# Performance work log

Hardware: AMD Instinct MI355X
Metric: run time of the kernel (lower is better)

The kernel has to match this reference:

```python
import jax, jax.numpy as jnp
import numpy as np
from jax import lax

K = 3          # kernel size
PAD = 1        # 'same' padding for k=3: (1,1,1,1)
STRIDE = 1
DIL = 1
OFFSET_SIZE = 2 * K * K  # deformable_groups=1


def setup_inputs() -> dict:
    key = jax.random.key(0)
    k1, k2, k3, k4 = jax.random.split(key, 4)
    B, H, W, C = 8, 64, 64, 256
    F = 256
    inputs = jax.random.normal(k1, (B, H, W, C), dtype=jnp.float32)
    # offset/mask branch conv: small weights so sampled offsets are modest
    om_kernel = jax.random.normal(k2, (K, K, C, OFFSET_SIZE * 3 // 2), dtype=jnp.float32) * 0.01
    om_bias = jnp.zeros((OFFSET_SIZE * 3 // 2,), dtype=jnp.float32)
    stdv = 1.0 / np.sqrt(K * K * C)
    kernel = jax.random.uniform(k3, (K * K * C, F), dtype=jnp.float32, minval=-stdv, maxval=stdv)
    bias = jax.random.normal(k4, (1, 1, 1, F), dtype=jnp.float32) * 0.01
    return {"inputs": inputs, "om_kernel": om_kernel, "om_bias": om_bias,
            "kernel": kernel, "bias": bias}


def _dcnv2(x, om_kernel, om_bias, kernel, bias):
    B, H, W, C = x.shape
    # offset/mask branch (same conv geometry as the deformable conv)
    om = lax.conv_general_dilated(
        x, om_kernel, window_strides=(STRIDE, STRIDE),
        padding=((PAD, PAD), (PAD, PAD)), rhs_dilation=(DIL, DIL),
        dimension_numbers=('NHWC', 'HWIO', 'NHWC')) + om_bias
    OH, OW = om.shape[1], om.shape[2]
    KK = K * K
    offset = om[..., :OFFSET_SIZE].reshape(B, OH, OW, KK, 2)  # (dy, dx) per kernel point
    mask = jax.nn.sigmoid(om[..., OFFSET_SIZE:]) * 2.0         # [B,OH,OW,KK]

    # base sampling grid per output pixel and kernel point
    kk = jnp.arange(KK)
    ky = (kk // K).astype(jnp.float32)
    kx = (kk % K).astype(jnp.float32)
    base_y = jnp.arange(OH, dtype=jnp.float32)[:, None] * STRIDE - PAD + ky[None, :] * DIL  # [OH,KK]
    base_x = jnp.arange(OW, dtype=jnp.float32)[:, None] * STRIDE - PAD + kx[None, :] * DIL  # [OW,KK]

    py = base_y[None, :, None, :] + offset[..., 0]  # [B,OH,OW,KK]
    px = base_x[None, None, :, :] + offset[..., 1]

    y0 = jnp.floor(py); x0 = jnp.floor(px)
    wy1 = py - y0; wy0 = 1.0 - wy1
    wx1 = px - x0; wx0 = 1.0 - wx1

    bi = jnp.arange(B)[:, None, None, None]

    def gather(yi, xi):
        # zero-padded bilinear corner fetch
        valid = (yi >= 0) & (yi <= H - 1) & (xi >= 0) & (xi <= W - 1)
        yc = jnp.clip(yi, 0, H - 1).astype(jnp.int32)
        xc = jnp.clip(xi, 0, W - 1).astype(jnp.int32)
        v = x[bi, yc, xc]  # [B,OH,OW,KK,C]
        return v * valid[..., None].astype(x.dtype)

    y1 = y0 + 1.0; x1 = x0 + 1.0
    cols = (gather(y0, x0) * (wy0 * wx0)[..., None]
            + gather(y0, x1) * (wy0 * wx1)[..., None]
            + gather(y1, x0) * (wy1 * wx0)[..., None]
            + gather(y1, x1) * (wy1 * wx1)[..., None])
    cols = cols * mask[..., None]  # modulation, [B,OH,OW,KK,C]

    out = cols.reshape(B, OH, OW, KK * C) @ kernel  # [B,OH,OW,F]
    return out + bias


def reference(inputs, om_kernel, om_bias, kernel, bias):
    return _dcnv2(inputs, om_kernel, om_bias, kernel, bias)
```

## Files before the change

kernel.cpp:

```cpp
#include <hip/hip_runtime.h>
#include <math.h>


#define BB 8
#define HH 64
#define WW 64
#define CIN 256
#define FF 256
#define KPTS 9
#define OCH 27
#define MT 32
#define KSTEPS 72
#define AST 40

typedef _Float16 half8  __attribute__((ext_vector_type(8)));
typedef _Float16 half4v __attribute__((ext_vector_type(4)));
typedef float    floatx4 __attribute__((ext_vector_type(4)));

__global__ __launch_bounds__(256) void convert_wmat(const float* __restrict__ wmat,
                                                    _Float16* __restrict__ wsB) {
    const int kg = blockIdx.x;
    const int n  = threadIdx.x;
    half8 h;
    #pragma unroll
    for (int j = 0; j < 8; ++j)
        h[j] = (_Float16)wmat[(size_t)(kg * 8 + j) * FF + n];
    ((half8*)wsB)[(size_t)kg * FF + n] = h;
}

__global__ __launch_bounds__(256) void convert_omw(const float* __restrict__ omw,
                                                   _Float16* __restrict__ wsOM) {
    const int t = blockIdx.x * 256 + threadIdx.x;
    const int k = t >> 5, n = t & 31;
    const float v = (n < OCH) ? omw[k * OCH + n] : 0.f;
    wsOM[((size_t)(k >> 3) * 32 + n) * 8 + (k & 7)] = (_Float16)v;
}

__global__ __launch_bounds__(256) void dcn_mfma(
    const float* __restrict__ x,
    const float* __restrict__ omb,
    const _Float16* __restrict__ wsB,
    const _Float16* __restrict__ wsOM,
    const float* __restrict__ bias,
    float* __restrict__ out)
{
    __shared__ _Float16 Ah0[MT * AST];
    __shared__ _Float16 Ah1[MT * AST];
    __shared__ float    om_s[MT][28];
    __shared__ floatx4  cwS[MT][KPTS];
    __shared__ int4     caS[MT][KPTS];

    const int tid  = threadIdx.x;
    const int w    = tid >> 6;
    const int lane = tid & 63;
    const int q    = lane >> 4;
    const int lr   = lane & 15;

    const int p   = blockIdx.x;
    const int b   = p & 7;
    const int r2  = p >> 3;
    const int oh  = r2 >> 1;
    const int owb = (r2 & 1) * 32;
    const int pbase = (b * HH + oh) * WW + owb;

    const int mrow = tid >> 3;
    const int cg   = tid & 7;

    const half8* wsOM8 = (const half8*)wsOM;
    const half8* wsB8  = (const half8*)wsB;

    const int mt1 = w & 1;
    const int nt1 = w >> 1;
    floatx4 acc1 = {0.f, 0.f, 0.f, 0.f};

    auto pre1 = [&](int s2, floatx4& cA, half8& bPre) {
        const int kk = s2 >> 3, cb = (s2 & 7) << 5;
        const int ky = kk / 3, kx = kk % 3;
        const int iy = oh - 1 + ky, ix = owb + mrow - 1 + kx;
        floatx4 v = {0.f, 0.f, 0.f, 0.f};
        if (iy >= 0 && iy < HH && ix >= 0 && ix < WW)
            v = *(const floatx4*)(x + ((size_t)((b * HH + iy) * WW + ix) * CIN + cb + cg * 4));
        cA = v;
        bPre = wsOM8[(s2 * 4 + q) * 32 + nt1 * 16 + lr];
    };

    floatx4 cA0, cA1;
    half8 bo0, bo1;
    pre1(0, cA0, bo0);
    for (int s = 0; s < KSTEPS; s += 2) {
        {
            half4v hv;
            hv.x = (_Float16)cA0.x; hv.y = (_Float16)cA0.y;
            hv.z = (_Float16)cA0.z; hv.w = (_Float16)cA0.w;
            *(half4v*)(&Ah0[mrow * AST + cg * 4]) = hv;
            pre1(s + 1, cA1, bo1);
            __syncthreads();
            const half8 a = *(const half8*)(&Ah0[(mt1 * 16 + lr) * AST + q * 8]);
            acc1 = __builtin_amdgcn_mfma_f32_16x16x32_f16(a, bo0, acc1, 0, 0, 0);
        }
        {
            half4v hv;
            hv.x = (_Float16)cA1.x; hv.y = (_Float16)cA1.y;
            hv.z = (_Float16)cA1.z; hv.w = (_Float16)cA1.w;
            *(half4v*)(&Ah1[mrow * AST + cg * 4]) = hv;
            const int s2 = (s + 2 < KSTEPS) ? s + 2 : KSTEPS - 1;
            pre1(s2, cA0, bo0);
            __syncthreads();
            const half8 a = *(const half8*)(&Ah1[(mt1 * 16 + lr) * AST + q * 8]);
            acc1 = __builtin_amdgcn_mfma_f32_16x16x32_f16(a, bo1, acc1, 0, 0, 0);
        }
    }
    {
        const int och = nt1 * 16 + lr;
        if (och < OCH) {
            const float ob = omb[och];
            #pragma unroll
            for (int reg = 0; reg < 4; ++reg) {
                const int m = mt1 * 16 + q * 4 + reg;
                om_s[m][och] = acc1[reg] + ob;
            }
        }
    }
    __syncthreads();

    for (int i = tid; i < MT * KPTS; i += 256) {
        const int m = i / KPTS, kk = i % KPTS;
        const int ky = kk / 3, kx = kk % 3;
        const float dy = om_s[m][2 * kk];
        const float dx = om_s[m][2 * kk + 1];
        const float mask = 2.f / (1.f + __expf(-om_s[m][18 + kk]));
        const float py = (float)(oh - 1 + ky) + dy;
        const float px = (float)(owb + m - 1 + kx) + dx;
        const float y0f = floorf(py), x0f = floorf(px);
        const float wy1 = py - y0f, wx1 = px - x0f;
        const float wy0 = 1.f - wy1, wx0 = 1.f - wx1;
        const int y0 = (int)y0f, x0 = (int)x0f;
        const int y1 = y0 + 1, x1 = x0 + 1;
        const bool vy0 = (y0 >= 0) && (y0 < HH);
        const bool vy1 = (y1 >= 0) && (y1 < HH);
        const bool vx0 = (x0 >= 0) && (x0 < WW);
        const bool vx1 = (x1 >= 0) && (x1 < WW);
        const int y0c = min(max(y0, 0), HH - 1), y1c = min(max(y1, 0), HH - 1);
        const int x0c = min(max(x0, 0), WW - 1), x1c = min(max(x1, 0), WW - 1);
        const int rb = b * HH;
        int4 ca;
        ca.x = ((rb + y0c) * WW + x0c) * CIN;
        ca.y = ((rb + y0c) * WW + x1c) * CIN;
        ca.z = ((rb + y1c) * WW + x0c) * CIN;
        ca.w = ((rb + y1c) * WW + x1c) * CIN;
        floatx4 cw;
        cw.x = (vy0 && vx0) ? mask * wy0 * wx0 : 0.f;
        cw.y = (vy0 && vx1) ? mask * wy0 * wx1 : 0.f;
        cw.z = (vy1 && vx0) ? mask * wy1 * wx0 : 0.f;
        cw.w = (vy1 && vx1) ? mask * wy1 * wx1 : 0.f;
        caS[m][kk] = ca;
        cwS[m][kk] = cw;
    }
    __syncthreads();

    floatx4 acc[2][4];
    #pragma unroll
    for (int mt = 0; mt < 2; ++mt)
        #pragma unroll
        for (int nt = 0; nt < 4; ++nt)
            acc[mt][nt] = (floatx4){0.f, 0.f, 0.f, 0.f};

    const int n0w = w * 64;

    auto pre2 = [&](int s2, floatx4& c0, floatx4& c1, floatx4& c2, floatx4& c3,
                    floatx4& cw, half8 (&bP)[4]) {
        const int kk2 = s2 >> 3;
        const int4 ca = caS[mrow][kk2];
        cw = cwS[mrow][kk2];
        const int co = ((s2 & 7) << 5) + cg * 4;
        c0 = *(const floatx4*)(x + ca.x + co);
        c1 = *(const floatx4*)(x + ca.y + co);
        c2 = *(const floatx4*)(x + ca.z + co);
        c3 = *(const floatx4*)(x + ca.w + co);
        #pragma unroll
        for (int nt = 0; nt < 4; ++nt)
            bP[nt] = wsB8[(s2 * 4 + q) * FF + n0w + nt * 16 + lr];
    };

    floatx4 ca0, ca1, ca2, ca3, cwa;
    floatx4 cb0, cb1, cb2, cb3, cwb;
    half8 bPa[4], bPb[4];
    pre2(0, ca0, ca1, ca2, ca3, cwa, bPa);

    for (int s = 0; s < KSTEPS; s += 2) {
        {
            const floatx4 v = cwa.x * ca0 + cwa.y * ca1 + cwa.z * ca2 + cwa.w * ca3;
            half4v hv;
            hv.x = (_Float16)v.x; hv.y = (_Float16)v.y;
            hv.z = (_Float16)v.z; hv.w = (_Float16)v.w;
            *(half4v*)(&Ah0[mrow * AST + cg * 4]) = hv;
            pre2(s + 1, cb0, cb1, cb2, cb3, cwb, bPb);
            __syncthreads();
            const half8 a0 = *(const half8*)(&Ah0[lr * AST + q * 8]);
            const half8 a1 = *(const half8*)(&Ah0[(16 + lr) * AST + q * 8]);
            #pragma unroll
            for (int nt = 0; nt < 4; ++nt) {
                acc[0][nt] = __builtin_amdgcn_mfma_f32_16x16x32_f16(a0, bPa[nt], acc[0][nt], 0, 0, 0);
                acc[1][nt] = __builtin_amdgcn_mfma_f32_16x16x32_f16(a1, bPa[nt], acc[1][nt], 0, 0, 0);
            }
        }
        {
            const floatx4 v = cwb.x * cb0 + cwb.y * cb1 + cwb.z * cb2 + cwb.w * cb3;
            half4v hv;
            hv.x = (_Float16)v.x; hv.y = (_Float16)v.y;
            hv.z = (_Float16)v.z; hv.w = (_Float16)v.w;
            *(half4v*)(&Ah1[mrow * AST + cg * 4]) = hv;
            const int s2 = (s + 2 < KSTEPS) ? s + 2 : KSTEPS - 1;
            pre2(s2, ca0, ca1, ca2, ca3, cwa, bPa);
            __syncthreads();
            const half8 a0 = *(const half8*)(&Ah1[lr * AST + q * 8]);
            const half8 a1 = *(const half8*)(&Ah1[(16 + lr) * AST + q * 8]);
            #pragma unroll
            for (int nt = 0; nt < 4; ++nt) {
                acc[0][nt] = __builtin_amdgcn_mfma_f32_16x16x32_f16(a0, bPb[nt], acc[0][nt], 0, 0, 0);
                acc[1][nt] = __builtin_amdgcn_mfma_f32_16x16x32_f16(a1, bPb[nt], acc[1][nt], 0, 0, 0);
            }
        }
    }

    #pragma unroll
    for (int nt = 0; nt < 4; ++nt) {
        const int f = n0w + nt * 16 + lr;
        const float bv = bias[f];
        #pragma unroll
        for (int mt = 0; mt < 2; ++mt)
            #pragma unroll
            for (int reg = 0; reg < 4; ++reg) {
                const int m = mt * 16 + q * 4 + reg;
                out[(size_t)(pbase + m) * FF + f] = acc[mt][nt][reg] + bv;
            }
    }
}

#define MTILE 32
#define CHUNK 64
#define NCHUNK (CIN / CHUNK)

__global__ __launch_bounds__(256) void dcn_fused(
    const float* __restrict__ x, const float* __restrict__ omw,
    const float* __restrict__ omb, const float* __restrict__ wmat,
    const float* __restrict__ bias, float* __restrict__ out)
{
    __shared__ float A[CHUNK][MTILE + 1];
    __shared__ float om_s[MTILE][28];
    __shared__ float cw[MTILE][4];
    __shared__ int   ca[MTILE][4];

    const int tid = threadIdx.x;
    const int pbase = blockIdx.x * MTILE;
    const int ccid = tid & 63;
    const int mg2 = tid >> 6;
    const int och = tid & 31;
    const int mg1 = tid >> 5;
    float acc1[4] = {0.f, 0.f, 0.f, 0.f};

    for (int kk = 0; kk < KPTS; ++kk) {
        const int ky = kk / 3, kx = kk % 3;
        for (int ch = 0; ch < NCHUNK; ++ch) {
            const int cbase = ch * CHUNK;
            __syncthreads();
            #pragma unroll
            for (int i = 0; i < 8; ++i) {
                const int m = mg2 * 8 + i;
                const int pp = pbase + m;
                const int bb = pp >> 12, oh = (pp >> 6) & 63, ow = pp & 63;
                const int iy = oh - 1 + ky, ix = ow - 1 + kx;
                float v = 0.f;
                if (iy >= 0 && iy < HH && ix >= 0 && ix < WW)
                    v = x[((bb * HH + iy) * WW + ix) * CIN + cbase + ccid];
                A[ccid][m] = v;
            }
            __syncthreads();
            if (och < OCH) {
                for (int cc = 0; cc < CHUNK; ++cc) {
                    const float bv = omw[((kk * CIN) + cbase + cc) * OCH + och];
                    #pragma unroll
                    for (int i = 0; i < 4; ++i)
                        acc1[i] += A[cc][mg1 * 4 + i] * bv;
                }
            }
        }
    }
    __syncthreads();
    if (och < OCH) {
        const float ob = omb[och];
        #pragma unroll
        for (int i = 0; i < 4; ++i)
            om_s[mg1 * 4 + i][och] = acc1[i] + ob;
    }
    __syncthreads();

    const int f4 = (tid & 63) * 4;
    const int mgc = tid >> 6;
    float acc[8][4];
    #pragma unroll
    for (int j = 0; j < 8; ++j)
        #pragma unroll
        for (int i = 0; i < 4; ++i) acc[j][i] = 0.f;

    for (int kk = 0; kk < KPTS; ++kk) {
        if (tid < MTILE) {
            const int m = tid;
            const int pp = pbase + m;
            const int bb = pp >> 12, oh = (pp >> 6) & 63, ow = pp & 63;
            const int ky = kk / 3, kx = kk % 3;
            const float dy = om_s[m][2 * kk];
            const float dx = om_s[m][2 * kk + 1];
            const float mask = 2.f / (1.f + __expf(-om_s[m][18 + kk]));
            const float py = (float)(oh - 1 + ky) + dy;
            const float px = (float)(ow - 1 + kx) + dx;
            const float y0f = floorf(py), x0f = floorf(px);
            const float wy1 = py - y0f, wx1 = px - x0f;
            const float wy0 = 1.f - wy1, wx0 = 1.f - wx1;
            const int y0 = (int)y0f, x0 = (int)x0f;
            const int y1 = y0 + 1, x1 = x0 + 1;
            const bool vy0 = (y0 >= 0) && (y0 < HH);
            const bool vy1 = (y1 >= 0) && (y1 < HH);
            const bool vx0 = (x0 >= 0) && (x0 < WW);
            const bool vx1 = (x1 >= 0) && (x1 < WW);
            const int y0c = min(max(y0, 0), HH - 1), y1c = min(max(y1, 0), HH - 1);
            const int x0c = min(max(x0, 0), WW - 1), x1c = min(max(x1, 0), WW - 1);
            const int rb = bb * HH;
            ca[m][0] = ((rb + y0c) * WW + x0c) * CIN;
            ca[m][1] = ((rb + y0c) * WW + x1c) * CIN;
            ca[m][2] = ((rb + y1c) * WW + x0c) * CIN;
            ca[m][3] = ((rb + y1c) * WW + x1c) * CIN;
            cw[m][0] = (vy0 && vx0) ? mask * wy0 * wx0 : 0.f;
            cw[m][1] = (vy0 && vx1) ? mask * wy0 * wx1 : 0.f;
            cw[m][2] = (vy1 && vx0) ? mask * wy1 * wx0 : 0.f;
            cw[m][3] = (vy1 && vx1) ? mask * wy1 * wx1 : 0.f;
        }
        for (int ch = 0; ch < NCHUNK; ++ch) {
            const int cbase = ch * CHUNK;
            __syncthreads();
            #pragma unroll
            for (int i = 0; i < 8; ++i) {
                const int m = mg2 * 8 + i;
                const int cidx = cbase + ccid;
                const float v = cw[m][0] * x[ca[m][0] + cidx]
                              + cw[m][1] * x[ca[m][1] + cidx]
                              + cw[m][2] * x[ca[m][2] + cidx]
                              + cw[m][3] * x[ca[m][3] + cidx];
                A[ccid][m] = v;
            }
            __syncthreads();
            const float* brow = wmat + (size_t)(kk * CIN + cbase) * FF + f4;
            for (int cc = 0; cc < CHUNK; ++cc) {
                const float4 bv = *(const float4*)(brow + cc * FF);
                #pragma unroll
                for (int j = 0; j < 8; ++j) {
                    const float a = A[cc][mgc * 8 + j];
                    acc[j][0] += a * bv.x;
                    acc[j][1] += a * bv.y;
                    acc[j][2] += a * bv.z;
                    acc[j][3] += a * bv.w;
                }
            }
        }
    }

    const float4 bb4 = *(const float4*)(bias + f4);
    #pragma unroll
    for (int j = 0; j < 8; ++j) {
        const int m = mgc * 8 + j;
        const int pp = pbase + m;
        float4 o;
        o.x = acc[j][0] + bb4.x;
        o.y = acc[j][1] + bb4.y;
        o.z = acc[j][2] + bb4.z;
        o.w = acc[j][3] + bb4.w;
        *(float4*)(out + (size_t)pp * FF + f4) = o;
    }
}

extern "C" void kernel_launch(void* const* d_in, const int* in_sizes, int n_in,
                              void* d_out, int out_size, void* d_ws, size_t ws_size,
                              hipStream_t stream) {
    const float* x    = (const float*)d_in[0];
    const float* omw  = (const float*)d_in[1];
    const float* omb  = (const float*)d_in[2];
    const float* wmat = (const float*)d_in[3];
    const float* bias = (const float*)d_in[4];
    float* out = (float*)d_out;

    const size_t needB  = (size_t)2304 * FF * sizeof(_Float16);
    const size_t needOM = (size_t)288 * 32 * 8 * sizeof(_Float16);

    if (ws_size >= needB + needOM) {
        _Float16* wsB  = (_Float16*)d_ws;
        _Float16* wsOM = (_Float16*)((char*)d_ws + needB);
        convert_wmat<<<288, 256, 0, stream>>>(wmat, wsB);
        convert_omw<<<288, 256, 0, stream>>>(omw, wsOM);
        dcn_mfma<<<BB * HH * 2, 256, 0, stream>>>(x, omb, wsB, wsOM, bias, out);
    } else {
        const int nblocks = (BB * HH * WW) / MTILE;
        dcn_fused<<<nblocks, 256, 0, stream>>>(x, omw, omb, wmat, bias, out);
    }
}
```

Before: 192.0 us.

## Use 512-thread full-row tiles with warp-group producer split, f16 input copy, swizzled LDS

Each block now covers a full output row of 64 pixels with 512 threads. The two 256-thread halves alternately fill the two LDS A buffers while all warps run MFMA, which lets gather latency overlap compute. A pre-pass converts x to fp16 in the workspace so the bilinear gathers fetch half the bytes, and the bilinear blend is done in fp16. LDS rows use an XOR swizzle instead of padding. The fp16 blending and weights lower accuracy, and the extra conversion pass of x adds a full read and write of the input.

```diff
diff --git a/kernel.cpp b/kernel.cpp
--- a/kernel.cpp
+++ b/kernel.cpp
@@ -9,13 +9,32 @@
 #define FF 256
 #define KPTS 9
 #define OCH 27
-#define MT 32
+#define MT 64
 #define KSTEPS 72
-#define AST 40
 
 typedef _Float16 half8  __attribute__((ext_vector_type(8)));
 typedef _Float16 half4v __attribute__((ext_vector_type(4)));
 typedef float    floatx4 __attribute__((ext_vector_type(4)));
+
+__device__ __forceinline__ int aoff(int m, int g) {
+    return m * 32 + ((g ^ ((m >> 1) & 3)) << 3);
+}
+
+__device__ __forceinline__ half8 splat8(_Float16 v) {
+    half8 r = {v, v, v, v, v, v, v, v};
+    return r;
+}
+
+__global__ __launch_bounds__(256) void convert_x(const float* __restrict__ x,
+                                                 _Float16* __restrict__ xh) {
+    const size_t i = ((size_t)blockIdx.x * 256 + threadIdx.x) * 8;
+    const floatx4 a = *(const floatx4*)(x + i);
+    const floatx4 b = *(const floatx4*)(x + i + 4);
+    half8 h;
+    h[0] = (_Float16)a.x; h[1] = (_Float16)a.y; h[2] = (_Float16)a.z; h[3] = (_Float16)a.w;
+    h[4] = (_Float16)b.x; h[5] = (_Float16)b.y; h[6] = (_Float16)b.z; h[7] = (_Float16)b.w;
+    *(half8*)(xh + i) = h;
+}
 
 __global__ __launch_bounds__(256) void convert_wmat(const float* __restrict__ wmat,
                                                     _Float16* __restrict__ wsB) {
@@ -36,18 +55,20 @@
     wsOM[((size_t)(k >> 3) * 32 + n) * 8 + (k & 7)] = (_Float16)v;
 }
 
-__global__ __launch_bounds__(256) void dcn_mfma(
+template <bool F16X>
+__global__ __launch_bounds__(512) void dcn_mfma2(
     const float* __restrict__ x,
+    const _Float16* __restrict__ xh,
     const float* __restrict__ omb,
     const _Float16* __restrict__ wsB,
     const _Float16* __restrict__ wsOM,
     const float* __restrict__ bias,
     float* __restrict__ out)
 {
-    __shared__ _Float16 Ah0[MT * AST];
-    __shared__ _Float16 Ah1[MT * AST];
+    __shared__ _Float16 Ah0[MT * 32];
+    __shared__ _Float16 Ah1[MT * 32];
     __shared__ float    om_s[MT][28];
-    __shared__ floatx4  cwS[MT][KPTS];
+    __shared__ half4v   cwS[MT][KPTS];
     __shared__ int4     caS[MT][KPTS];
 
     const int tid  = threadIdx.x;
@@ -55,58 +76,80 @@
     const int lane = tid & 63;
     const int q    = lane >> 4;
     const int lr   = lane & 15;
-
-    const int p   = blockIdx.x;
-    const int b   = p & 7;
-    const int r2  = p >> 3;
-    const int oh  = r2 >> 1;
-    const int owb = (r2 & 1) * 32;
-    const int pbase = (b * HH + oh) * WW + owb;
-
-    const int mrow = tid >> 3;
-    const int cg   = tid & 7;
+    const int g    = tid >> 8;
+    const int st   = tid & 255;
+    const int ms   = st >> 2;
+    const int qc   = st & 3;
+
+    const int p  = blockIdx.x;
+    const int b  = p & 7;
+    const int oh = p >> 3;
+    const int pbase = (b * HH + oh) * WW;
 
     const half8* wsOM8 = (const half8*)wsOM;
     const half8* wsB8  = (const half8*)wsB;
 
-    const int mt1 = w & 1;
-    const int nt1 = w >> 1;
+    const int mt1 = w & 3;
+    const int nt1 = w >> 2;
     floatx4 acc1 = {0.f, 0.f, 0.f, 0.f};
 
-    auto pre1 = [&](int s2, floatx4& cA, half8& bPre) {
-        const int kk = s2 >> 3, cb = (s2 & 7) << 5;
-        const int ky = kk / 3, kx = kk % 3;
-        const int iy = oh - 1 + ky, ix = owb + mrow - 1 + kx;
-        floatx4 v = {0.f, 0.f, 0.f, 0.f};
-        if (iy >= 0 && iy < HH && ix >= 0 && ix < WW)
-            v = *(const floatx4*)(x + ((size_t)((b * HH + iy) * WW + ix) * CIN + cb + cg * 4));
-        cA = v;
-        bPre = wsOM8[(s2 * 4 + q) * 32 + nt1 * 16 + lr];
+    auto load1 = [&](int sp) -> half8 {
+        sp = sp < KSTEPS - 1 ? sp : KSTEPS - 1;
+        const int kk = sp >> 3, cb = (sp & 7) << 5;
+        const int ky = kk / 3, kx = kk - ky * 3;
+        const int iy = oh - 1 + ky, ix = ms - 1 + kx;
+        half8 v = {(_Float16)0, (_Float16)0, (_Float16)0, (_Float16)0,
+                   (_Float16)0, (_Float16)0, (_Float16)0, (_Float16)0};
+        if (iy >= 0 && iy < HH && ix >= 0 && ix < WW) {
+            const int idx = ((b * HH + iy) * WW + ix) * CIN + cb + qc * 8;
+            if constexpr (F16X) {
+                v = *(const half8*)(xh + idx);
+            } else {
+                const floatx4 lo = *(const floatx4*)(x + idx);
+                const floatx4 hi = *(const floatx4*)(x + idx + 4);
+                v[0] = (_Float16)lo.x; v[1] = (_Float16)lo.y;
+                v[2] = (_Float16)lo.z; v[3] = (_Float16)lo.w;
+                v[4] = (_Float16)hi.x; v[5] = (_Float16)hi.y;
+                v[6] = (_Float16)hi.z; v[7] = (_Float16)hi.w;
+            }
+        }
+        return v;
     };
-
-    floatx4 cA0, cA1;
+    auto loadB1 = [&](int sp) -> half8 {
+        sp = sp < KSTEPS - 1 ? sp : KSTEPS - 1;
+        return wsOM8[(sp * 4 + q) * 32 + nt1 * 16 + lr];
+    };
+
+    half8 vp1;
     half8 bo0, bo1;
-    pre1(0, cA0, bo0);
+    if (g == 0) {
+        const half8 v0 = load1(0);
+        *(half8*)(Ah0 + aoff(ms, qc)) = v0;
+        vp1 = load1(2);
+    } else {
+        vp1 = load1(1);
+    }
+    bo0 = loadB1(0);
+
     for (int s = 0; s < KSTEPS; s += 2) {
+        __syncthreads();
+        if (g == 1) {
+            *(half8*)(Ah1 + aoff(ms, qc)) = vp1;
+            vp1 = load1(s + 3);
+        }
+        bo1 = loadB1(s + 1);
         {
-            half4v hv;
-            hv.x = (_Float16)cA0.x; hv.y = (_Float16)cA0.y;
-            hv.z = (_Float16)cA0.z; hv.w = (_Float16)cA0.w;
-            *(half4v*)(&Ah0[mrow * AST + cg * 4]) = hv;
-            pre1(s + 1, cA1, bo1);
-            __syncthreads();
-            const half8 a = *(const half8*)(&Ah0[(mt1 * 16 + lr) * AST + q * 8]);
+            const half8 a = *(const half8*)(Ah0 + aoff(mt1 * 16 + lr, q));
             acc1 = __builtin_amdgcn_mfma_f32_16x16x32_f16(a, bo0, acc1, 0, 0, 0);
         }
+        __syncthreads();
+        if (g == 0) {
+            *(half8*)(Ah0 + aoff(ms, qc)) = vp1;
+            vp1 = load1(s + 4);
+        }
+        bo0 = loadB1(s + 2);
         {
-            half4v hv;
-            hv.x = (_Float16)cA1.x; hv.y = (_Float16)cA1.y;
-            hv.z = (_Float16)cA1.z; hv.w = (_Float16)cA1.w;
-            *(half4v*)(&Ah1[mrow * AST + cg * 4]) = hv;
-            const int s2 = (s + 2 < KSTEPS) ? s + 2 : KSTEPS - 1;
-            pre1(s2, cA0, bo0);
-            __syncthreads();
-            const half8 a = *(const half8*)(&Ah1[(mt1 * 16 + lr) * AST + q * 8]);
+            const half8 a = *(const half8*)(Ah1 + aoff(mt1 * 16 + lr, q));
             acc1 = __builtin_amdgcn_mfma_f32_16x16x32_f16(a, bo1, acc1, 0, 0, 0);
         }
     }
@@ -123,14 +166,14 @@
     }
     __syncthreads();
 
-    for (int i = tid; i < MT * KPTS; i += 256) {
+    for (int i = tid; i < MT * KPTS; i += 512) {
         const int m = i / KPTS, kk = i % KPTS;
-        const int ky = kk / 3, kx = kk % 3;
+        const int ky = kk / 3, kx = kk - ky * 3;
         const float dy = om_s[m][2 * kk];
         const float dx = om_s[m][2 * kk + 1];
         const float mask = 2.f / (1.f + __expf(-om_s[m][18 + kk]));
         const float py = (float)(oh - 1 + ky) + dy;
-        const float px = (float)(owb + m - 1 + kx) + dx;
+        const float px = (float)(m - 1 + kx) + dx;
         const float y0f = floorf(py), x0f = floorf(px);
         const float wy1 = py - y0f, wx1 = px - x0f;
         const float wy0 = 1.f - wy1, wx0 = 1.f - wx1;
@@ -148,87 +191,129 @@
         ca.y = ((rb + y0c) * WW + x1c) * CIN;
         ca.z = ((rb + y1c) * WW + x0c) * CIN;
         ca.w = ((rb + y1c) * WW + x1c) * CIN;
-        floatx4 cw;
-        cw.x = (vy0 && vx0) ? mask * wy0 * wx0 : 0.f;
-        cw.y = (vy0 && vx1) ? mask * wy0 * wx1 : 0.f;
-        cw.z = (vy1 && vx0) ? mask * wy1 * wx0 : 0.f;
-        cw.w = (vy1 && vx1) ? mask * wy1 * wx1 : 0.f;
+        half4v cw;
+        cw.x = (_Float16)((vy0 && vx0) ? mask * wy0 * wx0 : 0.f);
+        cw.y = (_Float16)((vy0 && vx1) ? mask * wy0 * wx1 : 0.f);
+        cw.z = (_Float16)((vy1 && vx0) ? mask * wy1 * wx0 : 0.f);
+        cw.w = (_Float16)((vy1 && vx1) ? mask * wy1 * wx1 : 0.f);
         caS[m][kk] = ca;
         cwS[m][kk] = cw;
     }
     __syncthreads();
 
-    floatx4 acc[2][4];
+    floatx4 acc[4][2];
     #pragma unroll
-    for (int mt = 0; mt < 2; ++mt)
+    for (int mt = 0; mt < 4; ++mt)
         #pragma unroll
-        for (int nt = 0; nt < 4; ++nt)
+        for (int nt = 0; nt < 2; ++nt)
             acc[mt][nt] = (floatx4){0.f, 0.f, 0.f, 0.f};
 
-    const int n0w = w * 64;
-
-    auto pre2 = [&](int s2, floatx4& c0, floatx4& c1, floatx4& c2, floatx4& c3,
-                    floatx4& cw, half8 (&bP)[4]) {
-        const int kk2 = s2 >> 3;
-        const int4 ca = caS[mrow][kk2];
-        cw = cwS[mrow][kk2];
-        const int co = ((s2 & 7) << 5) + cg * 4;
-        c0 = *(const floatx4*)(x + ca.x + co);
-        c1 = *(const floatx4*)(x + ca.y + co);
-        c2 = *(const floatx4*)(x + ca.z + co);
-        c3 = *(const floatx4*)(x + ca.w + co);
+    const int n0w = w * 32;
+
+    half8   pc0, pc1, pc2, pc3;
+    floatx4 fa0, fb0, fa1, fb1, fa2, fb2, fa3, fb3;
+    half4v  pcw;
+
+    auto pre2 = [&](int sp) {
+        sp = sp < KSTEPS - 1 ? sp : KSTEPS - 1;
+        const int kk = sp >> 3;
+        const int co = ((sp & 7) << 5) + qc * 8;
+        const int4 ca = caS[ms][kk];
+        pcw = cwS[ms][kk];
+        if constexpr (F16X) {
+            pc0 = *(const half8*)(xh + ca.x + co);
+            pc1 = *(const half8*)(xh + ca.y + co);
+            pc2 = *(const half8*)(xh + ca.z + co);
+            pc3 = *(const half8*)(xh + ca.w + co);
+        } else {
+            fa0 = *(const floatx4*)(x + ca.x + co); fb0 = *(const floatx4*)(x + ca.x + co + 4);
+            fa1 = *(const floatx4*)(x + ca.y + co); fb1 = *(const floatx4*)(x + ca.y + co + 4);
+            fa2 = *(const floatx4*)(x + ca.z + co); fb2 = *(const floatx4*)(x + ca.z + co + 4);
+            fa3 = *(const floatx4*)(x + ca.w + co); fb3 = *(const floatx4*)(x + ca.w + co + 4);
+        }
+    };
+    auto comb = [&]() -> half8 {
+        if constexpr (F16X) {
+            const half8 w0 = splat8(pcw.x), w1 = splat8(pcw.y);
+            const half8 w2 = splat8(pcw.z), w3 = splat8(pcw.w);
+            return pc0 * w0 + pc1 * w1 + pc2 * w2 + pc3 * w3;
+        } else {
+            const float w0 = (float)pcw.x, w1 = (float)pcw.y;
+            const float w2 = (float)pcw.z, w3 = (float)pcw.w;
+            const floatx4 lo = w0 * fa0 + w1 * fa1 + w2 * fa2 + w3 * fa3;
+            const floatx4 hi = w0 * fb0 + w1 * fb1 + w2 * fb2 + w3 * fb3;
+            half8 r;
+            r[0] = (_Float16)lo.x; r[1] = (_Float16)lo.y;
+            r[2] = (_Float16)lo.z; r[3] = (_Float16)lo.w;
+            r[4] = (_Float16)hi.x; r[5] = (_Float16)hi.y;
+            r[6] = (_Float16)hi.z; r[7] = (_Float16)hi.w;
+            return r;
+        }
+    };
+
+    half8 bPa[2], bPb[2];
+    auto loadB2 = [&](int sp, half8 (&bP)[2]) {
+        sp = sp < KSTEPS - 1 ? sp : KSTEPS - 1;
         #pragma unroll
-        for (int nt = 0; nt < 4; ++nt)
-            bP[nt] = wsB8[(s2 * 4 + q) * FF + n0w + nt * 16 + lr];
+        for (int nt = 0; nt < 2; ++nt)
+            bP[nt] = wsB8[(size_t)(sp * 4 + q) * FF + n0w + nt * 16 + lr];
     };
 
-    floatx4 ca0, ca1, ca2, ca3, cwa;
-    floatx4 cb0, cb1, cb2, cb3, cwb;
-    half8 bPa[4], bPb[4];
-    pre2(0, ca0, ca1, ca2, ca3, cwa, bPa);
+    if (g == 0) {
+        pre2(0);
+        const half8 v0 = comb();
+        *(half8*)(Ah0 + aoff(ms, qc)) = v0;
+        pre2(2);
+    } else {
+        pre2(1);
+    }
+    loadB2(0, bPa);
 
     for (int s = 0; s < KSTEPS; s += 2) {
+        __syncthreads();
+        if (g == 1) {
+            const half8 v = comb();
+            *(half8*)(Ah1 + aoff(ms, qc)) = v;
+            pre2(s + 3);
+        }
+        loadB2(s + 1, bPb);
         {
-            const floatx4 v = cwa.x * ca0 + cwa.y * ca1 + cwa.z * ca2 + cwa.w * ca3;
-            half4v hv;
-            hv.x = (_Float16)v.x; hv.y = (_Float16)v.y;
-            hv.z = (_Float16)v.z; hv.w = (_Float16)v.w;
-            *(half4v*)(&Ah0[mrow * AST + cg * 4]) = hv;
-            pre2(s + 1, cb0, cb1, cb2, cb3, cwb, bPb);
-            __syncthreads();
-            const half8 a0 = *(const half8*)(&Ah0[lr * AST + q * 8]);
-            const half8 a1 = *(const half8*)(&Ah0[(16 + lr) * AST + q * 8]);
-            #pragma unroll
-            for (int nt = 0; nt < 4; ++nt) {
-                acc[0][nt] = __builtin_amdgcn_mfma_f32_16x16x32_f16(a0, bPa[nt], acc[0][nt], 0, 0, 0);
-                acc[1][nt] = __builtin_amdgcn_mfma_f32_16x16x32_f16(a1, bPa[nt], acc[1][nt], 0, 0, 0);
-            }
-        }
+            half8 afr[4];
+            #pragma unroll
+            for (int mt = 0; mt < 4; ++mt)
+                afr[mt] = *(const half8*)(Ah0 + aoff(mt * 16 + lr, q));
+            #pragma unroll
+            for (int nt = 0; nt < 2; ++nt)
+                #pragma unroll
+                for (int mt = 0; mt < 4; ++mt)
+                    acc[mt][nt] = __builtin_amdgcn_mfma_f32_16x16x32_f16(afr[mt], bPa[nt], acc[mt][nt], 0, 0, 0);
+        }
+        __syncthreads();
+        if (g == 0) {
+            const half8 v = comb();
+            *(half8*)(Ah0 + aoff(ms, qc)) = v;
+            pre2(s + 4);
+        }
+        loadB2(s + 2, bPa);
         {
-            const floatx4 v = cwb.x * cb0 + cwb.y * cb1 + cwb.z * cb2 + cwb.w * cb3;
-            half4v hv;
-            hv.x = (_Float16)v.x; hv.y = (_Float16)v.y;
-            hv.z = (_Float16)v.z; hv.w = (_Float16)v.w;
-            *(half4v*)(&Ah1[mrow * AST + cg * 4]) = hv;
-            const int s2 = (s + 2 < KSTEPS) ? s + 2 : KSTEPS - 1;
-            pre2(s2, ca0, ca1, ca2, ca3, cwa, bPa);
-            __syncthreads();
-            const half8 a0 = *(const half8*)(&Ah1[lr * AST + q * 8]);
-            const half8 a1 = *(const half8*)(&Ah1[(16 + lr) * AST + q * 8]);
-            #pragma unroll
-            for (int nt = 0; nt < 4; ++nt) {
-                acc[0][nt] = __builtin_amdgcn_mfma_f32_16x16x32_f16(a0, bPb[nt], acc[0][nt], 0, 0, 0);
-                acc[1][nt] = __builtin_amdgcn_mfma_f32_16x16x32_f16(a1, bPb[nt], acc[1][nt], 0, 0, 0);
-            }
+            half8 afr[4];
+            #pragma unroll
+            for (int mt = 0; mt < 4; ++mt)
+                afr[mt] = *(const half8*)(Ah1 + aoff(mt * 16 + lr, q));
+            #pragma unroll
+            for (int nt = 0; nt < 2; ++nt)
+                #pragma unroll
+                for (int mt = 0; mt < 4; ++mt)
+                    acc[mt][nt] = __builtin_amdgcn_mfma_f32_16x16x32_f16(afr[mt], bPb[nt], acc[mt][nt], 0, 0, 0);
         }
     }
 
     #pragma unroll
-    for (int nt = 0; nt < 4; ++nt) {
+    for (int nt = 0; nt < 2; ++nt) {
         const int f = n0w + nt * 16 + lr;
         const float bv = bias[f];
         #pragma unroll
-        for (int mt = 0; mt < 2; ++mt)
+        for (int mt = 0; mt < 4; ++mt)
             #pragma unroll
             for (int reg = 0; reg < 4; ++reg) {
                 const int m = mt * 16 + q * 4 + reg;
@@ -390,13 +475,22 @@
 
     const size_t needB  = (size_t)2304 * FF * sizeof(_Float16);
     const size_t needOM = (size_t)288 * 32 * 8 * sizeof(_Float16);
-
-    if (ws_size >= needB + needOM) {
+    const size_t needX  = (size_t)BB * HH * WW * CIN * sizeof(_Float16);
+
+    if (ws_size >= needB + needOM + needX) {
+        _Float16* wsB  = (_Float16*)d_ws;
+        _Float16* wsOM = (_Float16*)((char*)d_ws + needB);
+        _Float16* xh   = (_Float16*)((char*)d_ws + needB + needOM);
+        convert_x<<<(BB * HH * WW * CIN) / (256 * 8), 256, 0, stream>>>(x, xh);
+        convert_wmat<<<288, 256, 0, stream>>>(wmat, wsB);
+        convert_omw<<<288, 256, 0, stream>>>(omw, wsOM);
+        dcn_mfma2<true><<<BB * HH, 512, 0, stream>>>(x, xh, omb, wsB, wsOM, bias, out);
+    } else if (ws_size >= needB + needOM) {
         _Float16* wsB  = (_Float16*)d_ws;
         _Float16* wsOM = (_Float16*)((char*)d_ws + needB);
         convert_wmat<<<288, 256, 0, stream>>>(wmat, wsB);
         convert_omw<<<288, 256, 0, stream>>>(omw, wsOM);
-        dcn_mfma<<<BB * HH * 2, 256, 0, stream>>>(x, omb, wsB, wsOM, bias, out);
+        dcn_mfma2<false><<<BB * HH, 512, 0, stream>>>(x, nullptr, omb, wsB, wsOM, bias, out);
     } else {
         const int nblocks = (BB * HH * WW) / MTILE;
         dcn_fused<<<nblocks, 256, 0, stream>>>(x, omw, omb, wmat, bias, out);
```

After: 170.1 us. 11.4% less time.
